# Performance work log

Measured on AMD Instinct MI355X. Metric: run time of the kernel, lower is better.

Reference implementation:

```python
import jax, jax.numpy as jnp
import numpy as np
from jax import lax

B, T, D, H, W = 2, 8, 64, 64, 64
E, HID = 4, 256


def _layernorm(x, g, b, eps=1e-5):
    m = x.mean(-1, keepdims=True)
    v = ((x - m) ** 2).mean(-1, keepdims=True)
    return (x - m) / jnp.sqrt(v + eps) * g + b


def _pscan(A, X, axis):
    # linear recurrence h_t = A_t * h_{t-1} + X_t via associative scan
    def comb(l, r):
        a1, x1 = l
        a2, x2 = r
        return a2 * a1, a2 * x1 + x2
    return lax.associative_scan(comb, (A, X), axis=axis)[1]


def setup_inputs() -> dict:
    key = jax.random.key(0)
    ks = jax.random.split(key, 32)
    r = lambda i, shape, s=1.0: jax.random.normal(ks[i], shape, jnp.float32) * s
    D2 = 2 * D
    return {
        'x_re': r(0, (B, T, D, H, W)), 'x_im': r(1, (B, T, D, H, W)),
        'dt': jax.random.uniform(ks[2], (T,), jnp.float32, 0.5, 1.0),
        'ln_s_g': jnp.ones(D2), 'ln_s_b': jnp.zeros(D2),
        'conv_w': r(3, (3, 3, D2, D2), 0.03), 'conv_b': jnp.zeros(D2),
        'mom_w': r(4, (D2, D2), 0.08), 'mom_b': jnp.zeros(D2),
        'adv_w': jnp.full((1,), 0.1, jnp.float32),
        'enc_re': r(5, (D, D), 0.1), 'enc_im': r(6, (D, D), 0.1),
        'dec_re': r(7, (D, D), 0.1), 'dec_im': r(8, (D, D), 0.1),
        'flux_a_re': r(9, (D,)), 'flux_a_im': r(10, (D,), 0.1),
        'fin_re': r(11, (D, D), 0.1), 'fin_im': r(12, (D, D), 0.1),
        'fproj_re': r(13, (D, D), 0.1), 'fproj_im': r(14, (D, D), 0.1),
        'gate_w': r(15, (D2, D), 0.1), 'gate_b': jnp.zeros(D),
        'lam_re': r(16, (D,)), 'lam_im': r(17, (D,), 0.1),
        'noise_re': r(18, (B, T, H, W, D)), 'noise_im': r(19, (B, T, H, W, D)),
        'e_scale': jnp.full((1,), 0.1, jnp.float32),
        'ln_t_g': jnp.ones(D2), 'ln_t_b': jnp.zeros(D2),
        'router_w': r(20, (D2, E), 0.1), 'router_b': jnp.zeros(E),
        'w1': r(21, (E, D2, HID), 0.08), 'b1': jnp.zeros((E, HID)),
        'w2': r(22, (E, HID, D2), 0.08), 'b2': jnp.zeros((E, D2)),
    }


def _forward(x_re, x_im, dt, ln_s_g, ln_s_b, conv_w, conv_b, mom_w, mom_b, adv_w,
             enc_re, enc_im, dec_re, dec_im, flux_a_re, flux_a_im, fin_re, fin_im,
             fproj_re, fproj_im, gate_w, gate_b, lam_re, lam_im, noise_re, noise_im,
             e_scale, ln_t_g, ln_t_b, router_w, router_b, w1, b1, w2, b2):
    x = (x_re + 1j * x_im).astype(jnp.complex64)            # [B,T,D,H,W]
    target_energy = (jnp.abs(x) ** 2).mean(axis=(-2, -1))   # [B,T,D]
    momentum = x.mean(axis=(-2, -1))                        # [B,T,D] complex
    xcl = jnp.transpose(x, (0, 1, 3, 4, 2))                 # [B,T,H,W,D]
    Bs, Ts, Hs, Ws, Ds = xcl.shape
    D2 = 2 * Ds
    # --- spatial complex (Clifford) conv branch: LN over 2D channels + conv ---
    xr = jnp.concatenate([xcl.real, xcl.imag], -1)          # [B,T,H,W,2D]
    xn = _layernorm(xr, ln_s_g, ln_s_b)
    y = lax.conv_general_dilated(xn.reshape(Bs * Ts, Hs, Ws, D2), conv_w,
                                 (1, 1), 'SAME',
                                 dimension_numbers=('NHWC', 'HWIO', 'NHWC')) + conv_b
    y = y.reshape(Bs, Ts, Hs, Ws, D2)
    xcl = xcl + (y[..., :Ds] + 1j * y[..., Ds:])
    # --- momentum advection ---
    z_mean = xcl.mean(axis=(2, 3))                          # [B,T,D]
    mom_cat = jnp.concatenate([momentum.real, momentum.imag], -1) @ mom_w + mom_b
    mom_new = mom_cat[..., :Ds] + 1j * mom_cat[..., Ds:]
    dtb = jnp.broadcast_to(dt[None, :], (Bs, Ts))
    xcl = xcl + (mom_new * adv_w[0])[:, :, None, None, :] * dtb[:, :, None, None, None]
    momentum = 0.9 * momentum + 0.1 * z_mean
    # --- eigenbasis encode ---
    x_eigen = xcl @ (enc_re + 1j * enc_im)                  # [B,T,H,W,D]
    x_mean = x_eigen.mean(axis=(2, 3))                      # [B,T,D]
    # --- flux tracker: parallel scan over T ---
    A_flux = jnp.exp(-jax.nn.softplus(flux_a_re) + 1j * flux_a_im)
    A_flux = jnp.broadcast_to(A_flux, (Bs, Ts, Ds)).astype(jnp.complex64)
    X_flux = x_mean @ (fin_re + 1j * fin_im)
    flux_seq = _pscan(A_flux, X_flux, axis=1)               # [B,T,D]
    source = flux_seq @ (fproj_re + 1j * fproj_im)
    gate = jax.nn.sigmoid(jnp.concatenate([flux_seq.real, flux_seq.imag], -1) @ gate_w + gate_b)
    g = gate[:, :, None, None, :]
    forcing = x_eigen * g + source[:, :, None, None, :] * (1.0 - g)
    # --- temporal propagation: per-site parallel scan over T ---
    lam = -jax.nn.softplus(lam_re) + 1j * lam_im            # [D]
    op_decay = jnp.exp(lam[None, None, :] * dtb[:, :, None])  # [B,T,D]
    op_forcing = (op_decay - 1.0) / lam
    u_t = forcing * op_forcing[:, :, None, None, :]
    A_time = jnp.broadcast_to(op_decay[:, :, None, None, :], u_t.shape)
    u_out = _pscan(A_time, u_t, axis=1)                     # [B,T,H,W,D]
    noise = 0.01 * jnp.sqrt(dtb)[:, :, None, None, None] * (noise_re + 1j * noise_im)
    u_out = u_out + noise
    # --- decode + energy projection ---
    x_out = u_out @ (dec_re + 1j * dec_im)                  # [B,T,H,W,D]
    cur_e = (jnp.abs(x_out) ** 2).mean(axis=(2, 3))
    ratio = jnp.clip(target_energy / (cur_e + 1e-8), 0.5, 2.0)
    sf = jnp.sqrt(ratio)[:, :, None, None, :]
    x_out = x_out * (1.0 + e_scale[0] * (sf - 1.0))
    # --- temporal LN + MoE FFN on real-concat tokens ---
    xr2 = jnp.concatenate([x_out.real, x_out.imag], -1)
    xn2 = _layernorm(xr2, ln_t_g, ln_t_b)                   # [B,T,H,W,2D]
    tok = xn2.reshape(-1, D2)                               # [N,2D]
    p = jax.nn.softmax(tok @ router_w + router_b, -1)       # [N,E]
    hmid = jax.nn.gelu(jnp.einsum('nd,edh->neh', tok, w1) + b1)
    eout = jnp.einsum('neh,ehd->ned', hmid, w2) + b2
    out_tok = tok + jnp.einsum('ne,ned->nd', p, eout)
    out = out_tok.reshape(Bs, Ts, Hs, Ws, D2)
    x_out_c = out[..., :Ds] + 1j * out[..., Ds:]
    z_out = xcl + x_out_c
    z = jnp.transpose(z_out, (0, 1, 4, 2, 3))               # [B,T,D,H,W]
    return jnp.stack([z.real, z.imag])                      # [2,B,T,D,H,W]


def reference(x_re, x_im, dt, ln_s_g, ln_s_b, conv_w, conv_b, mom_w, mom_b, adv_w,
              enc_re, enc_im, dec_re, dec_im, flux_a_re, flux_a_im, fin_re, fin_im,
              fproj_re, fproj_im, gate_w, gate_b, lam_re, lam_im, noise_re, noise_im,
              e_scale, ln_t_g, ln_t_b, router_w, router_b, w1, b1, w2, b2):
    return _forward(x_re, x_im, dt, ln_s_g, ln_s_b, conv_w, conv_b, mom_w, mom_b, adv_w,
                    enc_re, enc_im, dec_re, dec_im, flux_a_re, flux_a_im, fin_re, fin_im,
                    fproj_re, fproj_im, gate_w, gate_b, lam_re, lam_im, noise_re, noise_im,
                    e_scale, ln_t_g, ln_t_b, router_w, router_b, w1, b1, w2, b2)
```

## Files before the change

kernel.cpp:

```cpp
#include <hip/hip_runtime.h>
#include <hip/hip_bf16.h>
#include <math.h>


#define W_C      8388608u
#define W_CWT    12582912u
#define W_W1T    14680064u
#define W_W2T    14745600u
#define W_ENCM   14811136u
#define W_DECM   14819328u
#define W_XMP_RE 14827520u
#define W_XMP_IM 14893056u
#define W_EP_RE  14958592u
#define W_EP_IM  15220736u
#define W_EIG_RE 16777216u
#define W_K1R    20971520u
#define W_K1I    21037056u
#define W_K1E    21102592u
#define W_SMALL  25165824u
#define W_TE     (W_SMALL+0u)
#define W_MTRE   (W_SMALL+3072u)
#define W_MTIM   (W_SMALL+4096u)
#define W_GATE   (W_SMALL+5120u)
#define W_SRCRE  (W_SMALL+6144u)
#define W_SRCIM  (W_SMALL+7168u)
#define W_OPFRE  (W_SMALL+8192u)
#define W_OPFIM  (W_SMALL+9216u)
#define W_OPDRE  (W_SMALL+10240u)
#define W_OPDIM  (W_SMALL+11264u)
#define W_SCALE  (W_SMALL+12288u)

#define XB_IM 4194304u

typedef __attribute__((ext_vector_type(8))) short bf16x8;
typedef __attribute__((ext_vector_type(4))) float f32x4;

__device__ __forceinline__ unsigned short bfr(float x) {
  __hip_bfloat16 h = __float2bfloat16(x);
  return *(unsigned short*)&h;
}
__device__ __forceinline__ unsigned int pk2(float a, float b) {
  return ((unsigned int)bfr(b) << 16) | (unsigned int)bfr(a);
}
__device__ __forceinline__ float sb2f(short s) {
  return __uint_as_float(((unsigned int)(unsigned short)s) << 16);
}

__global__ __launch_bounds__(256) void k2_transpose_ln(
    const float* __restrict__ xre, const float* __restrict__ xim,
    const float* __restrict__ g, const float* __restrict__ bb_, float* ws) {
  int blk = blockIdx.x; int bt = blk >> 6, h = blk & 63;
  __shared__ float tre[64][65], tim[64][65];
  __shared__ float ps[4][64], pq[4][64], pe[4][64];
  __shared__ float mean_l[64], rstd_l[64];
  size_t inbase = (size_t)bt * 262144 + (size_t)h * 64;
  for (int i = threadIdx.x; i < 1024; i += 256) {
    int d = i >> 4, w4 = (i & 15) * 4;
    float4 vr = *(const float4*)&xre[inbase + (size_t)d * 4096 + w4];
    float4 vi = *(const float4*)&xim[inbase + (size_t)d * 4096 + w4];
    tre[d][w4] = vr.x; tre[d][w4 + 1] = vr.y; tre[d][w4 + 2] = vr.z; tre[d][w4 + 3] = vr.w;
    tim[d][w4] = vi.x; tim[d][w4 + 1] = vi.y; tim[d][w4 + 2] = vi.z; tim[d][w4 + 3] = vi.w;
  }
  __syncthreads();
  {
    int w = threadIdx.x & 63, part = threadIdx.x >> 6;
    float s = 0.f, sq = 0.f;
    for (int dd = part * 16; dd < part * 16 + 16; dd++) {
      float vr = tre[dd][w], vi = tim[dd][w];
      s += vr + vi; sq += vr * vr + vi * vi;
    }
    ps[part][w] = s; pq[part][w] = sq;
  }
  __syncthreads();
  if (threadIdx.x < 64) {
    int w = threadIdx.x;
    float s  = ps[0][w] + ps[1][w] + ps[2][w] + ps[3][w];
    float sq = pq[0][w] + pq[1][w] + pq[2][w] + pq[3][w];
    float m = s / 128.f;
    float v = sq / 128.f - m * m;
    mean_l[w] = m; rstd_l[w] = rsqrtf(v + 1e-5f);
  }
  __syncthreads();
  {
    int d = threadIdx.x & 63, part = threadIdx.x >> 6;
    float sr = 0.f, si = 0.f, se = 0.f;
    for (int w = part * 16; w < part * 16 + 16; w++) {
      float vr = tre[d][w], vi = tim[d][w];
      sr += vr; si += vi; se += vr * vr + vi * vi;
    }
    ps[part][d] = sr; pq[part][d] = si; pe[part][d] = se;
  }
  __syncthreads();
  if (threadIdx.x < 64) {
    int d = threadIdx.x;
    int idx = h * 1024 + bt * 64 + d;
    ws[W_K1R + idx] = ps[0][d] + ps[1][d] + ps[2][d] + ps[3][d];
    ws[W_K1I + idx] = pq[0][d] + pq[1][d] + pq[2][d] + pq[3][d];
    ws[W_K1E + idx] = pe[0][d] + pe[1][d] + pe[2][d] + pe[3][d];
  }
  size_t tokbase = (size_t)blk * 64;
  __hip_bfloat16* xnb = (__hip_bfloat16*)(ws + W_C);
  int c0 = (threadIdx.x & 63) * 2, wg = threadIdx.x >> 6;
  float gc0 = g[c0], bc0 = bb_[c0], gc1 = g[c0 + 1], bc1 = bb_[c0 + 1];
  for (int pass = 0; pass < 16; pass++) {
    int w = pass * 4 + wg;
    float m = mean_l[w], rs = rstd_l[w];
    float v0 = (c0 < 64) ? tre[c0][w] : tim[c0 - 64][w];
    float v1 = (c0 + 1 < 64) ? tre[c0 + 1][w] : tim[c0 + 1 - 64][w];
    *(unsigned int*)&xnb[tokbase * 128 + (size_t)w * 128 + c0] =
        pk2((v0 - m) * rs * gc0 + bc0, (v1 - m) * rs * gc1 + bc1);
  }
}

__global__ void k1b2b(const float* __restrict__ mom_w, const float* __restrict__ mom_b,
                      const float* __restrict__ adv_w, const float* __restrict__ dt, float* ws) {
  int bt = blockIdx.x; int t = bt & 7;
  __shared__ float mc[128], outl[128];
  int tid = threadIdx.x;
  if (tid < 64) {
    int d = tid;
    float a = 0.f, b = 0.f, c = 0.f;
    for (int h = 0; h < 64; h++) {
      int idx = h * 1024 + bt * 64 + d;
      a += ws[W_K1R + idx]; b += ws[W_K1I + idx]; c += ws[W_K1E + idx];
    }
    ws[W_TE + bt * 64 + d] = c / 4096.f;
    mc[d] = a / 4096.f;
    mc[64 + d] = b / 4096.f;
  }
  __syncthreads();
  float acc = mom_b[tid];
  for (int k = 0; k < 128; k++) acc += mc[k] * mom_w[k * 128 + tid];
  outl[tid] = acc;
  __syncthreads();
  if (tid < 64) {
    float f = adv_w[0] * dt[t];
    ws[W_MTRE + bt * 64 + tid] = outl[tid] * f;
    ws[W_MTIM + bt * 64 + tid] = outl[64 + tid] * f;
  }
}

__global__ void k0_wprep(const float* __restrict__ w1, const float* __restrict__ w2,
                         const float* __restrict__ cw,
                         const float* __restrict__ enc_re, const float* __restrict__ enc_im,
                         const float* __restrict__ dec_re, const float* __restrict__ dec_im,
                         float* ws) {
  __hip_bfloat16* w1f = (__hip_bfloat16*)(ws + W_W1T);
  __hip_bfloat16* w2f = (__hip_bfloat16*)(ws + W_W2T);
  __hip_bfloat16* cwt = (__hip_bfloat16*)(ws + W_CWT);
  __hip_bfloat16* encM = (__hip_bfloat16*)(ws + W_ENCM);
  __hip_bfloat16* decM = (__hip_bfloat16*)(ws + W_DECM);
  int idx = blockIdx.x * 256 + threadIdx.x;
  if (idx < 131072) {
    {
      int j = idx & 7, lane = (idx >> 3) & 63, kt = (idx >> 9) & 3, nt = (idx >> 11) & 15, e = idx >> 15;
      int cout = nt * 16 + (lane & 15);
      int cin = kt * 32 + (lane >> 4) * 8 + j;
      w1f[idx] = __float2bfloat16(w1[((size_t)(e * 128 + cin)) * 256 + cout]);
    }
    {
      int j = idx & 7, lane = (idx >> 3) & 63, kt = (idx >> 9) & 7, nt = (idx >> 12) & 7, e = idx >> 15;
      int cout = nt * 16 + (lane & 15);
      int cin = kt * 32 + (lane >> 4) * 8 + j;
      w2f[idx] = __float2bfloat16(w2[((size_t)(e * 256 + cin)) * 128 + cout]);
    }
  }
  if (idx < 147456) {
    int j = idx & 7, lane = (idx >> 3) & 63, kt = (idx >> 9) & 3, r = idx >> 11;
    int nt = r & 7, tap = r >> 3;
    int cout = nt * 16 + (lane & 15);
    int cin = kt * 32 + (lane >> 4) * 8 + j;
    cwt[idx] = __float2bfloat16(cw[((size_t)(tap * 128 + cin)) * 128 + cout]);
  }
  if (idx < 16384) {
    int jj = idx & 7, lane = (idx >> 3) & 63, kt = (idx >> 9) & 3, nt = idx >> 11;
    int jc = nt * 16 + (lane & 15);
    int k = kt * 32 + (lane >> 4) * 8 + jj;
    float ve, vd;
    if (k < 64) {
      ve = (jc < 64) ? enc_re[k * 64 + jc] : enc_im[k * 64 + (jc - 64)];
      vd = (jc < 64) ? dec_re[k * 64 + jc] : dec_im[k * 64 + (jc - 64)];
    } else {
      int kk = k - 64;
      ve = (jc < 64) ? -enc_im[kk * 64 + jc] : enc_re[kk * 64 + (jc - 64)];
      vd = (jc < 64) ? -dec_im[kk * 64 + jc] : dec_re[kk * 64 + (jc - 64)];
    }
    encM[idx] = __float2bfloat16(ve);
    decM[idx] = __float2bfloat16(vd);
  }
}

__global__ __launch_bounds__(256) void k3_conv_enc(
    const float* __restrict__ xre, const float* __restrict__ xim,
    const float* __restrict__ cb, float* ws) {
  int blk = blockIdx.x; int bt = blk >> 6, h = blk & 63;
  const __hip_bfloat16* xnb = (const __hip_bfloat16*)(ws + W_C);
  const __hip_bfloat16* cwt = (const __hip_bfloat16*)(ws + W_CWT);
  const __hip_bfloat16* encM = (const __hip_bfloat16*)(ws + W_ENCM);
  __hip_bfloat16* xclb = (__hip_bfloat16*)ws;
  __hip_bfloat16* eigb = (__hip_bfloat16*)(ws + W_EIG_RE);
  __shared__ __align__(16) char smem[3 * 66 * 136 * 2];
  __hip_bfloat16 (*xin)[66][136] = (__hip_bfloat16(*)[66][136])smem;
  char* A = smem;
  int tid = threadIdx.x, lane = tid & 63, wv = tid >> 6;
  int arow = lane & 15, kgrp = (lane >> 4) * 8, rbase = (lane >> 4) * 4;

  for (int r = 0; r < 3; r++) {
    int hh = h + r - 1;
    if (hh < 0 || hh >= 64) {
      unsigned int* z = (unsigned int*)&xin[r][0][0];
      for (int i = tid; i < 4488; i += 256) z[i] = 0u;
    } else {
      if (tid < 68) *(unsigned int*)&xin[r][0][tid * 2] = 0u;
      else if (tid < 136) *(unsigned int*)&xin[r][65][(tid - 136 + 68) * 2] = 0u;
      const __hip_bfloat16* src = xnb + ((size_t)bt * 4096 + (size_t)hh * 64) * 128;
      for (int i = tid; i < 1024; i += 256) {
        int wp = (i >> 4) + 1, c8 = (i & 15) * 8;
        *(bf16x8*)&xin[r][wp][c8] = *(const bf16x8*)&src[(size_t)(wp - 1) * 128 + c8];
      }
    }
  }
  __syncthreads();

  f32x4 oacc[4][2];
  #pragma unroll
  for (int m = 0; m < 4; m++) {
    oacc[m][0] = (f32x4){0.f, 0.f, 0.f, 0.f};
    oacc[m][1] = (f32x4){0.f, 0.f, 0.f, 0.f};
  }

  for (int tap = 0; tap < 9; tap++) {
    int kh = tap / 3, kw = tap % 3;
    const __hip_bfloat16* wt0 = cwt + ((size_t)(tap * 8 + wv * 2) * 4) * 512 + lane * 8;
    #pragma unroll
    for (int kt = 0; kt < 4; kt++) {
      bf16x8 a[4];
      #pragma unroll
      for (int m = 0; m < 4; m++)
        a[m] = *(const bf16x8*)&xin[kh][m * 16 + arow + kw][kt * 32 + kgrp];
      bf16x8 b0 = *(const bf16x8*)&wt0[(size_t)kt * 512];
      bf16x8 b1 = *(const bf16x8*)&wt0[(size_t)(kt + 4) * 512];
      #pragma unroll
      for (int m = 0; m < 4; m++) {
        oacc[m][0] = __builtin_amdgcn_mfma_f32_16x16x32_bf16(a[m], b0, oacc[m][0], 0, 0, 0);
        oacc[m][1] = __builtin_amdgcn_mfma_f32_16x16x32_bf16(a[m], b1, oacc[m][1], 0, 0, 0);
      }
    }
  }
  __syncthreads();

  size_t rowtok = (size_t)blk * 64;
  #pragma unroll
  for (int n = 0; n < 2; n++) {
    int cout = (wv * 2 + n) * 16 + arow;
    bool isre = cout < 64;
    int d = cout & 63;
    float add = cb[cout] + ws[(isre ? W_MTRE : W_MTIM) + bt * 64 + d];
    size_t xb = isre ? 0u : XB_IM;
    const float* xsrc = (isre ? xre : xim) + ((size_t)(bt * 64 + d) * 64 + h) * 64;
    #pragma unroll
    for (int m = 0; m < 4; m++) {
      float4 xv = *(const float4*)&xsrc[m * 16 + rbase];
      #pragma unroll
      for (int r = 0; r < 4; r++) {
        int w = m * 16 + rbase + r;
        float xo = (r == 0) ? xv.x : (r == 1) ? xv.y : (r == 2) ? xv.z : xv.w;
        float v = xo + oacc[m][n][r] + add;
        xclb[xb + (rowtok + w) * 64 + d] = __float2bfloat16(v);
        *(__hip_bfloat16*)(A + w * 256 + ((cout * 2) ^ ((w & 7) << 4))) = __float2bfloat16(v);
      }
    }
  }
  __syncthreads();

  f32x4 acc[4][2];
  #pragma unroll
  for (int m = 0; m < 4; m++) {
    acc[m][0] = (f32x4){0.f, 0.f, 0.f, 0.f};
    acc[m][1] = (f32x4){0.f, 0.f, 0.f, 0.f};
  }
  #pragma unroll
  for (int kt = 0; kt < 4; kt++) {
    bf16x8 a[4];
    #pragma unroll
    for (int m = 0; m < 4; m++)
      a[m] = *(const bf16x8*)(A + (m * 16 + arow) * 256 + (((kt * 32 + kgrp) * 2) ^ ((arow & 7) << 4)));
    bf16x8 b0 = *(const bf16x8*)&encM[(((size_t)(wv * 2 + 0) * 4 + kt) * 64 + lane) * 8];
    bf16x8 b1 = *(const bf16x8*)&encM[(((size_t)(wv * 2 + 1) * 4 + kt) * 64 + lane) * 8];
    #pragma unroll
    for (int m = 0; m < 4; m++) {
      acc[m][0] = __builtin_amdgcn_mfma_f32_16x16x32_bf16(a[m], b0, acc[m][0], 0, 0, 0);
      acc[m][1] = __builtin_amdgcn_mfma_f32_16x16x32_bf16(a[m], b1, acc[m][1], 0, 0, 0);
    }
  }
  #pragma unroll
  for (int n = 0; n < 2; n++) {
    int jc = (wv * 2 + n) * 16 + arow;
    size_t eb = (jc < 64) ? 0u : XB_IM;
    int col = jc & 63;
    #pragma unroll
    for (int m = 0; m < 4; m++)
      #pragma unroll
      for (int r = 0; r < 4; r++)
        eigb[eb + (rowtok + m * 16 + rbase + r) * 64 + col] = __float2bfloat16(acc[m][n][r]);
    float s = 0.f;
    #pragma unroll
    for (int m = 0; m < 4; m++)
      #pragma unroll
      for (int r = 0; r < 4; r++) s += acc[m][n][r];
    s += __shfl_xor(s, 16);
    s += __shfl_xor(s, 32);
    if (lane < 16)
      ws[(jc < 64 ? W_XMP_RE : W_XMP_IM) + (size_t)blk * 64 + col] = s;
  }
}

__device__ __forceinline__ float softplusf(float x) {
  return (x > 20.f) ? x : log1pf(expf(x));
}

__global__ void k6_seq(const float* __restrict__ fin_re, const float* __restrict__ fin_im,
                       const float* __restrict__ fproj_re, const float* __restrict__ fproj_im,
                       const float* __restrict__ flux_a_re, const float* __restrict__ flux_a_im,
                       const float* __restrict__ gate_w, const float* __restrict__ gate_b,
                       const float* __restrict__ lam_re, const float* __restrict__ lam_im,
                       const float* __restrict__ dt, float* ws) {
  __shared__ float xmr[1024], xmi[1024], Xfr[1024], Xfi[1024], flr[1024], fli[1024];
  int tid = threadIdx.x;
  for (int i = tid; i < 1024; i += 256) {
    int bt = i >> 6, j = i & 63;
    float sr = 0.f, si = 0.f;
    for (int q = 0; q < 64; q++) {
      sr += ws[W_XMP_RE + (size_t)(bt * 64 + q) * 64 + j];
      si += ws[W_XMP_IM + (size_t)(bt * 64 + q) * 64 + j];
    }
    xmr[i] = sr / 4096.f; xmi[i] = si / 4096.f;
  }
  __syncthreads();
  for (int i = tid; i < 1024; i += 256) {
    int bt = i >> 6, j = i & 63;
    float ar = 0.f, ai = 0.f;
    for (int d = 0; d < 64; d++) {
      float xr = xmr[bt * 64 + d], xi = xmi[bt * 64 + d];
      float wr = fin_re[d * 64 + j], wi = fin_im[d * 64 + j];
      ar += xr * wr - xi * wi; ai += xr * wi + xi * wr;
    }
    Xfr[i] = ar; Xfi[i] = ai;
  }
  __syncthreads();
  if (tid < 128) {
    int b = tid >> 6, j = tid & 63;
    float mag = expf(-softplusf(flux_a_re[j]));
    float aar = mag * cosf(flux_a_im[j]), aai = mag * sinf(flux_a_im[j]);
    float sr = 0.f, si = 0.f;
    for (int t = 0; t < 8; t++) {
      int idx = (b * 8 + t) * 64 + j;
      float nr = aar * sr - aai * si + Xfr[idx];
      float ni = aar * si + aai * sr + Xfi[idx];
      sr = nr; si = ni;
      flr[idx] = sr; fli[idx] = si;
    }
  }
  __syncthreads();
  for (int i = tid; i < 1024; i += 256) {
    int bt = i >> 6, j = i & 63;
    float ar = 0.f, ai = 0.f, lg = 0.f;
    for (int d = 0; d < 64; d++) {
      float fr = flr[bt * 64 + d], fi = fli[bt * 64 + d];
      float wr = fproj_re[d * 64 + j], wi = fproj_im[d * 64 + j];
      ar += fr * wr - fi * wi; ai += fr * wi + fi * wr;
      lg += fr * gate_w[d * 64 + j] + fi * gate_w[(64 + d) * 64 + j];
    }
    ws[W_SRCRE + i] = ar; ws[W_SRCIM + i] = ai;
    ws[W_GATE + i] = 1.f / (1.f + expf(-(lg + gate_b[j])));
  }
  for (int i = tid; i < 1024; i += 256) {
    int bt = i >> 6, d = i & 63, t = bt & 7;
    float lr = -softplusf(lam_re[d]), li = lam_im[d];
    float dtv = dt[t];
    float mag = expf(lr * dtv);
    float dr = mag * cosf(li * dtv), di = mag * sinf(li * dtv);
    ws[W_OPDRE + i] = dr; ws[W_OPDIM + i] = di;
    float omr = dr - 1.f, omi = di;
    float den = lr * lr + li * li;
    ws[W_OPFRE + i] = (omr * lr + omi * li) / den;
    ws[W_OPFIM + i] = (omi * lr - omr * li) / den;
  }
}

__global__ __launch_bounds__(256) void k7_dec(const float* __restrict__ nre,
                                              const float* __restrict__ nim,
                                              const float* __restrict__ dt, float* ws) {
  int blk = blockIdx.x;
  int b = blk >> 8, h = (blk >> 2) & 63, wq = blk & 3;
  const __hip_bfloat16* decM = (const __hip_bfloat16*)(ws + W_DECM);
  __hip_bfloat16* eigb = (__hip_bfloat16*)(ws + W_EIG_RE);
  __shared__ float gl[8][64], srl[8][64], sil[8][64], ofr[8][64], ofi[8][64], odr[8][64], odi[8][64];
  __shared__ __align__(16) char A[2][4096];
  __shared__ float dts[8];
  int tid = threadIdx.x, lane = tid & 63, wv = tid >> 6;
  int arow = lane & 15, kgrp = (lane >> 4) * 8, rbase = (lane >> 4) * 4;
  for (int i = tid; i < 512; i += 256) {
    int t = i >> 6, d = i & 63, idx = (b * 8 + t) * 64 + d;
    gl[t][d]  = ws[W_GATE + idx];
    srl[t][d] = ws[W_SRCRE + idx]; sil[t][d] = ws[W_SRCIM + idx];
    ofr[t][d] = ws[W_OPFRE + idx]; ofi[t][d] = ws[W_OPFIM + idx];
    odr[t][d] = ws[W_OPDRE + idx]; odi[t][d] = ws[W_OPDIM + idx];
  }
  if (tid < 8) dts[tid] = dt[tid];
  __syncthreads();

  int dp = (tid & 31) * 2, wslot = tid >> 5;
  float ur[2][2], ui[2][2];
  #pragma unroll
  for (int a_ = 0; a_ < 2; a_++) { ur[a_][0] = 0.f; ur[a_][1] = 0.f; ui[a_][0] = 0.f; ui[a_][1] = 0.f; }

  for (int t = 0; t < 8; t++) {
    float ns = 0.01f * sqrtf(dts[t]);
    size_t tokb = ((size_t)(b * 8 + t) * 64 + h) * 64 + (size_t)wq * 16;
    char* At = A[t & 1];
    float g0 = gl[t][dp],  g1 = gl[t][dp + 1];
    float s0 = srl[t][dp], s1 = srl[t][dp + 1];
    float q0 = sil[t][dp], q1 = sil[t][dp + 1];
    float f0 = ofr[t][dp], f1 = ofr[t][dp + 1];
    float e0 = ofi[t][dp], e1 = ofi[t][dp + 1];
    float r0 = odr[t][dp], r1 = odr[t][dp + 1];
    float o0 = odi[t][dp], o1 = odi[t][dp + 1];
    #pragma unroll
    for (int wi = 0; wi < 2; wi++) {
      int wl = wslot + wi * 8;
      size_t off = (tokb + wl) * 64 + dp;
      unsigned int re2 = *(const unsigned int*)&eigb[off];
      unsigned int im2 = *(const unsigned int*)&eigb[XB_IM + off];
      float2 nr2 = *(const float2*)&nre[off];
      float2 ni2 = *(const float2*)&nim[off];
      float uo0, vo0, uo1, vo1;
      {
        float er_ = __uint_as_float(re2 << 16);
        float ei_ = __uint_as_float(im2 << 16);
        float fre = er_ * g0 + s0 * (1.f - g0);
        float fim = ei_ * g0 + q0 * (1.f - g0);
        float utr = fre * f0 - fim * e0;
        float uti = fre * e0 + fim * f0;
        float nur = r0 * ur[wi][0] - o0 * ui[wi][0] + utr;
        float nui = r0 * ui[wi][0] + o0 * ur[wi][0] + uti;
        ur[wi][0] = nur; ui[wi][0] = nui;
        uo0 = nur + ns * nr2.x; vo0 = nui + ns * ni2.x;
      }
      {
        float er_ = __uint_as_float(re2 & 0xffff0000u);
        float ei_ = __uint_as_float(im2 & 0xffff0000u);
        float fre = er_ * g1 + s1 * (1.f - g1);
        float fim = ei_ * g1 + q1 * (1.f - g1);
        float utr = fre * f1 - fim * e1;
        float uti = fre * e1 + fim * f1;
        float nur = r1 * ur[wi][1] - o1 * ui[wi][1] + utr;
        float nui = r1 * ui[wi][1] + o1 * ur[wi][1] + uti;
        ur[wi][1] = nur; ui[wi][1] = nui;
        uo1 = nur + ns * nr2.y; vo1 = nui + ns * ni2.y;
      }
      int sw = (wl & 7) << 4;
      *(unsigned int*)(At + wl * 256 + ((dp * 2) ^ sw)) = pk2(uo0, uo1);
      *(unsigned int*)(At + wl * 256 + ((128 + dp * 2) ^ sw)) = pk2(vo0, vo1);
    }
    __syncthreads();
    f32x4 acc[2];
    acc[0] = (f32x4){0.f, 0.f, 0.f, 0.f};
    acc[1] = (f32x4){0.f, 0.f, 0.f, 0.f};
    #pragma unroll
    for (int kt = 0; kt < 4; kt++) {
      bf16x8 a0 = *(const bf16x8*)(At + arow * 256 + (((kt * 32 + kgrp) * 2) ^ ((arow & 7) << 4)));
      bf16x8 b0 = *(const bf16x8*)&decM[(((size_t)(wv * 2 + 0) * 4 + kt) * 64 + lane) * 8];
      bf16x8 b1 = *(const bf16x8*)&decM[(((size_t)(wv * 2 + 1) * 4 + kt) * 64 + lane) * 8];
      acc[0] = __builtin_amdgcn_mfma_f32_16x16x32_bf16(a0, b0, acc[0], 0, 0, 0);
      acc[1] = __builtin_amdgcn_mfma_f32_16x16x32_bf16(a0, b1, acc[1], 0, 0, 0);
    }
    #pragma unroll
    for (int n = 0; n < 2; n++) {
      int jc = (wv * 2 + n) * 16 + arow;
      size_t eb = (jc < 64) ? 0u : XB_IM;
      int col = jc & 63;
      #pragma unroll
      for (int r = 0; r < 4; r++)
        eigb[eb + (tokb + rbase + r) * 64 + col] = __float2bfloat16(acc[n][r]);
      float s = acc[n][0] * acc[n][0] + acc[n][1] * acc[n][1]
              + acc[n][2] * acc[n][2] + acc[n][3] * acc[n][3];
      s += __shfl_xor(s, 16);
      s += __shfl_xor(s, 32);
      if (lane < 16)
        ws[(jc < 64 ? W_EP_RE : W_EP_IM)
           + (size_t)((b * 8 + t) * 256 + h * 4 + wq) * 64 + col] = s;
    }
  }
}

__global__ void k9b_scale(const float* __restrict__ escale, float* ws) {
  int bt = blockIdx.x; int j = threadIdx.x;
  float s = 0.f;
  for (int q = 0; q < 256; q++) {
    size_t idx = (size_t)(bt * 256 + q) * 64 + j;
    s += ws[W_EP_RE + idx] + ws[W_EP_IM + idx];
  }
  float cur = s / 4096.f;
  float te = ws[W_TE + bt * 64 + j];
  float ratio = te / (cur + 1e-8f);
  ratio = fminf(fmaxf(ratio, 0.5f), 2.0f);
  ws[W_SCALE + bt * 64 + j] = 1.f + escale[0] * (sqrtf(ratio) - 1.f);
}

__global__ __launch_bounds__(512) void k11_moe(
    const float* __restrict__ rw, const float* __restrict__ rb,
    const float* __restrict__ b1, const float* __restrict__ b2,
    const float* __restrict__ g2, const float* __restrict__ b2_,
    float* __restrict__ ws, float* __restrict__ out) {
  int blk = blockIdx.x; int bt = blk >> 6, h = blk & 63;
  const __hip_bfloat16* w1f = (const __hip_bfloat16*)(ws + W_W1T);
  const __hip_bfloat16* w2f = (const __hip_bfloat16*)(ws + W_W2T);
  const __hip_bfloat16* xclb = (const __hip_bfloat16*)ws;
  const __hip_bfloat16* eigb = (const __hip_bfloat16*)(ws + W_EIG_RE);
  __shared__ __align__(16) char smem[81920];
  __shared__ float pl[64][4];
  __shared__ float sc[64];
  __shared__ float mean_l[64], rstd_l[64];
  char* lt = smem;
  float (*obuf)[129] = (float(*)[129])smem;
  float* psq = (float*)(smem + 16384);
  int tid = threadIdx.x, lane = tid & 63, wv = tid >> 6;
  int arow = lane & 15, kgrp = (lane >> 4) * 8, rbase = (lane >> 4) * 4;
  size_t tokbase = (size_t)blk * 64;

  if (tid < 64) sc[tid] = ws[W_SCALE + bt * 64 + tid];
  __syncthreads();

  int w = tid >> 3, part = tid & 7;
  int c0 = part * 16, dbase = (part & 3) * 16;
  const __hip_bfloat16* rp = eigb + ((part < 4) ? 0u : XB_IM) + (tokbase + w) * 64 + dbase;
  float4 vv[4];
  {
    bf16x8 h0 = *(const bf16x8*)rp;
    bf16x8 h1 = *(const bf16x8*)(rp + 8);
    float f[16];
    #pragma unroll
    for (int j = 0; j < 8; j++) { f[j] = sb2f(h0[j]); f[8 + j] = sb2f(h1[j]); }
    float s = 0.f, sq = 0.f;
    #pragma unroll
    for (int q = 0; q < 4; q++) {
      float4 t4;
      t4.x = f[q * 4 + 0] * sc[dbase + q * 4 + 0];
      t4.y = f[q * 4 + 1] * sc[dbase + q * 4 + 1];
      t4.z = f[q * 4 + 2] * sc[dbase + q * 4 + 2];
      t4.w = f[q * 4 + 3] * sc[dbase + q * 4 + 3];
      vv[q] = t4;
      s  += t4.x + t4.y + t4.z + t4.w;
      sq += t4.x * t4.x + t4.y * t4.y + t4.z * t4.z + t4.w * t4.w;
    }
    psq[part * 64 + w] = s;
    psq[512 + part * 64 + w] = sq;
  }
  __syncthreads();
  if (tid < 64) {
    float s = 0.f, sq = 0.f;
    #pragma unroll
    for (int p = 0; p < 8; p++) { s += psq[p * 64 + tid]; sq += psq[512 + p * 64 + tid]; }
    float m = s / 128.f, v = sq / 128.f - m * m;
    mean_l[tid] = m; rstd_l[tid] = rsqrtf(v + 1e-5f);
  }
  __syncthreads();
  {
    float m = mean_l[w], rs = rstd_l[w];
    int szw = (w & 7) << 4;
    #pragma unroll
    for (int q = 0; q < 4; q++) {
      int c = c0 + q * 4;
      float a0 = (vv[q].x - m) * rs * g2[c]     + b2_[c];
      float a1 = (vv[q].y - m) * rs * g2[c + 1] + b2_[c + 1];
      float a2 = (vv[q].z - m) * rs * g2[c + 2] + b2_[c + 2];
      float a3 = (vv[q].w - m) * rs * g2[c + 3] + b2_[c + 3];
      *(unsigned int*)(lt + w * 256 + ((c * 2) ^ szw)) = pk2(a0, a1);
      *(unsigned int*)(lt + w * 256 + (((c + 2) * 2) ^ szw)) = pk2(a2, a3);
    }
  }
  __syncthreads();
  if (tid < 256) {
    int l = tid >> 2, e = tid & 3;
    float acc = rb[e];
    const float* rwe = rw + e;
    int sz = (l & 7) << 4;
    for (int dd = 0; dd < 128; dd += 2) {
      unsigned int u = *(const unsigned int*)(lt + l * 256 + ((dd * 2) ^ sz));
      float x0 = __uint_as_float(u << 16);
      float x1 = __uint_as_float(u & 0xffff0000u);
      acc += x0 * rwe[dd * 4] + x1 * rwe[dd * 4 + 4];
    }
    pl[l][e] = acc;
  }
  __syncthreads();
  if (tid < 64) {
    float m = fmaxf(fmaxf(pl[tid][0], pl[tid][1]), fmaxf(pl[tid][2], pl[tid][3]));
    float e0 = expf(pl[tid][0] - m), e1 = expf(pl[tid][1] - m);
    float e2 = expf(pl[tid][2] - m), e3 = expf(pl[tid][3] - m);
    float s = e0 + e1 + e2 + e3;
    float rs = __builtin_amdgcn_rcpf(s);
    pl[tid][0] = e0 * rs; pl[tid][1] = e1 * rs; pl[tid][2] = e2 * rs; pl[tid][3] = e3 * rs;
  }

  f32x4 oacc[4];
  #pragma unroll
  for (int m = 0; m < 4; m++) {
    int col = wv * 16 + arow;
    oacc[m] = (f32x4){0.f, 0.f, 0.f, 0.f};
    #pragma unroll
    for (int r = 0; r < 4; r++) {
      int row = m * 16 + rbase + r;
      oacc[m][r] = __bfloat162float(
          *(const __hip_bfloat16*)(lt + row * 256 + ((col * 2) ^ ((row & 7) << 4))));
    }
  }
  __syncthreads();

  for (int e = 0; e < 4; e++) {
    char* hb = smem + 16384 + (e & 1) * 32768;
    f32x4 acc1[4][2];
    #pragma unroll
    for (int m = 0; m < 4; m++) {
      acc1[m][0] = (f32x4){0.f, 0.f, 0.f, 0.f};
      acc1[m][1] = (f32x4){0.f, 0.f, 0.f, 0.f};
    }
    #pragma unroll
    for (int kt = 0; kt < 4; kt++) {
      bf16x8 a[4];
      #pragma unroll
      for (int m = 0; m < 4; m++) {
        int row = m * 16 + arow;
        a[m] = *(const bf16x8*)(lt + row * 256 + (((kt * 32 + kgrp) * 2) ^ ((arow & 7) << 4)));
      }
      bf16x8 b0 = *(const bf16x8*)&w1f[(((size_t)(e * 16 + wv * 2 + 0) * 4 + kt) * 64 + lane) * 8];
      bf16x8 b1 = *(const bf16x8*)&w1f[(((size_t)(e * 16 + wv * 2 + 1) * 4 + kt) * 64 + lane) * 8];
      #pragma unroll
      for (int m = 0; m < 4; m++) {
        acc1[m][0] = __builtin_amdgcn_mfma_f32_16x16x32_bf16(a[m], b0, acc1[m][0], 0, 0, 0);
        acc1[m][1] = __builtin_amdgcn_mfma_f32_16x16x32_bf16(a[m], b1, acc1[m][1], 0, 0, 0);
      }
    }
    #pragma unroll
    for (int n = 0; n < 2; n++) {
      int col = (wv * 2 + n) * 16 + arow;
      float bv = b1[e * 256 + col];
      #pragma unroll
      for (int m = 0; m < 4; m++)
        #pragma unroll
        for (int r = 0; r < 4; r++) {
          float hv = acc1[m][n][r] + bv;
          float z = 1.5957691216f * hv + 0.0713548162f * hv * hv * hv;
          float gelu = hv * __builtin_amdgcn_rcpf(1.f + __expf(-z));
          int row = m * 16 + rbase + r;
          *(__hip_bfloat16*)(hb + row * 512 + ((col * 2) ^ ((row & 7) << 4))) =
              __float2bfloat16(gelu);
        }
    }
    __syncthreads();
    f32x4 acc2[4];
    #pragma unroll
    for (int m = 0; m < 4; m++) acc2[m] = (f32x4){0.f, 0.f, 0.f, 0.f};
    #pragma unroll
    for (int kt = 0; kt < 8; kt++) {
      bf16x8 a2[4];
      #pragma unroll
      for (int m = 0; m < 4; m++) {
        int row = m * 16 + arow;
        a2[m] = *(const bf16x8*)(hb + row * 512 + (((kt * 32 + kgrp) * 2) ^ ((arow & 7) << 4)));
      }
      bf16x8 bb = *(const bf16x8*)&w2f[(((size_t)(e * 8 + wv) * 8 + kt) * 64 + lane) * 8];
      #pragma unroll
      for (int m = 0; m < 4; m++)
        acc2[m] = __builtin_amdgcn_mfma_f32_16x16x32_bf16(a2[m], bb, acc2[m], 0, 0, 0);
    }
    {
      int col = wv * 16 + arow;
      float bv2 = b2[e * 128 + col];
      #pragma unroll
      for (int m = 0; m < 4; m++)
        #pragma unroll
        for (int r = 0; r < 4; r++)
          oacc[m][r] += pl[m * 16 + rbase + r][e] * (acc2[m][r] + bv2);
    }
  }

  __syncthreads();
  #pragma unroll
  for (int m = 0; m < 4; m++) {
    int col = wv * 16 + arow;
    #pragma unroll
    for (int r = 0; r < 4; r++)
      obuf[m * 16 + rbase + r][col] = oacc[m][r];
  }
  __syncthreads();

  for (int i = tid; i < 4096; i += 512) {
    int wt = i >> 6, c0r = (i & 63) * 2;
    size_t xb = (c0r < 64) ? 0u : XB_IM;
    int dd = c0r & 63;
    unsigned int u = *(const unsigned int*)&xclb[xb + (tokbase + wt) * 64 + dd];
    obuf[wt][c0r]     += __uint_as_float(u << 16);
    obuf[wt][c0r + 1] += __uint_as_float(u & 0xffff0000u);
  }
  __syncthreads();
  for (int i = tid; i < 8192; i += 512) {
    int d2 = i >> 6, wt = i & 63;
    out[(size_t)(d2 >> 6) * 4194304 + (size_t)bt * 262144 + (size_t)(d2 & 63) * 4096
        + (size_t)h * 64 + wt] = obuf[wt][d2];
  }
}

extern "C" void kernel_launch(void* const* d_in, const int* in_sizes, int n_in,
                              void* d_out, int out_size, void* d_ws, size_t ws_size,
                              hipStream_t stream) {
  const float* x_re      = (const float*)d_in[0];
  const float* x_im      = (const float*)d_in[1];
  const float* dt        = (const float*)d_in[2];
  const float* ln_s_g    = (const float*)d_in[3];
  const float* ln_s_b    = (const float*)d_in[4];
  const float* conv_w    = (const float*)d_in[5];
  const float* conv_b    = (const float*)d_in[6];
  const float* mom_w     = (const float*)d_in[7];
  const float* mom_b     = (const float*)d_in[8];
  const float* adv_w     = (const float*)d_in[9];
  const float* enc_re    = (const float*)d_in[10];
  const float* enc_im    = (const float*)d_in[11];
  const float* dec_re    = (const float*)d_in[12];
  const float* dec_im    = (const float*)d_in[13];
  const float* flux_a_re = (const float*)d_in[14];
  const float* flux_a_im = (const float*)d_in[15];
  const float* fin_re    = (const float*)d_in[16];
  const float* fin_im    = (const float*)d_in[17];
  const float* fproj_re  = (const float*)d_in[18];
  const float* fproj_im  = (const float*)d_in[19];
  const float* gate_w    = (const float*)d_in[20];
  const float* gate_b    = (const float*)d_in[21];
  const float* lam_re    = (const float*)d_in[22];
  const float* lam_im    = (const float*)d_in[23];
  const float* noise_re  = (const float*)d_in[24];
  const float* noise_im  = (const float*)d_in[25];
  const float* e_scale   = (const float*)d_in[26];
  const float* ln_t_g    = (const float*)d_in[27];
  const float* ln_t_b    = (const float*)d_in[28];
  const float* router_w  = (const float*)d_in[29];
  const float* router_b  = (const float*)d_in[30];
  const float* w1        = (const float*)d_in[31];
  const float* b1        = (const float*)d_in[32];
  const float* w2        = (const float*)d_in[33];
  const float* b2        = (const float*)d_in[34];
  float* ws  = (float*)d_ws;
  float* out = (float*)d_out;

  k0_wprep<<<576, 256, 0, stream>>>(w1, w2, conv_w, enc_re, enc_im, dec_re, dec_im, ws);
  k2_transpose_ln<<<1024, 256, 0, stream>>>(x_re, x_im, ln_s_g, ln_s_b, ws);
  k1b2b<<<16, 128, 0, stream>>>(mom_w, mom_b, adv_w, dt, ws);
  k3_conv_enc<<<1024, 256, 0, stream>>>(x_re, x_im, conv_b, ws);
  k6_seq<<<1, 256, 0, stream>>>(fin_re, fin_im, fproj_re, fproj_im, flux_a_re, flux_a_im,
                                gate_w, gate_b, lam_re, lam_im, dt, ws);
  k7_dec<<<512, 256, 0, stream>>>(noise_re, noise_im, dt, ws);
  k9b_scale<<<16, 64, 0, stream>>>(e_scale, ws);
  k11_moe<<<1024, 512, 0, stream>>>(router_w, router_b, b1, b2, ln_t_g, ln_t_b, ws, out);
}
```

Measured before the change: 243.3 us.

## Fuse layernorm and router via wave shuffles; write MoE output directly from registers

Reads the per-channel scale straight from global memory and reduces the layernorm statistics and the router logits with xor-shuffles across the 8 threads that share a token. This removes the shared-memory partial-sum buffers and several block-wide barriers, and the softmax is computed redundantly in registers. The epilogue adds the bf16 residual per lane and stores float4 results straight to global memory, dropping the shared-memory transpose buffer and its barriers. In exchange the residual reads are scattered 2-byte gathers, and the barrier after the initial oacc read is removed. That removal relies on the first expert's writes landing in a different smem region than lt.

```diff
diff --git a/kernel.cpp b/kernel.cpp
--- a/kernel.cpp
+++ b/kernel.cpp
@@ -520,89 +520,64 @@
   const __hip_bfloat16* eigb = (const __hip_bfloat16*)(ws + W_EIG_RE);
   __shared__ __align__(16) char smem[81920];
   __shared__ float pl[64][4];
-  __shared__ float sc[64];
-  __shared__ float mean_l[64], rstd_l[64];
   char* lt = smem;
-  float (*obuf)[129] = (float(*)[129])smem;
-  float* psq = (float*)(smem + 16384);
   int tid = threadIdx.x, lane = tid & 63, wv = tid >> 6;
   int arow = lane & 15, kgrp = (lane >> 4) * 8, rbase = (lane >> 4) * 4;
   size_t tokbase = (size_t)blk * 64;
 
-  if (tid < 64) sc[tid] = ws[W_SCALE + bt * 64 + tid];
-  __syncthreads();
-
   int w = tid >> 3, part = tid & 7;
   int c0 = part * 16, dbase = (part & 3) * 16;
   const __hip_bfloat16* rp = eigb + ((part < 4) ? 0u : XB_IM) + (tokbase + w) * 64 + dbase;
-  float4 vv[4];
+  const float* scg = ws + W_SCALE + bt * 64 + dbase;
+  float an[16];
   {
     bf16x8 h0 = *(const bf16x8*)rp;
     bf16x8 h1 = *(const bf16x8*)(rp + 8);
     float f[16];
     #pragma unroll
-    for (int j = 0; j < 8; j++) { f[j] = sb2f(h0[j]); f[8 + j] = sb2f(h1[j]); }
+    for (int j = 0; j < 8; j++) {
+      f[j]     = sb2f(h0[j]) * scg[j];
+      f[8 + j] = sb2f(h1[j]) * scg[8 + j];
+    }
     float s = 0.f, sq = 0.f;
     #pragma unroll
-    for (int q = 0; q < 4; q++) {
-      float4 t4;
-      t4.x = f[q * 4 + 0] * sc[dbase + q * 4 + 0];
-      t4.y = f[q * 4 + 1] * sc[dbase + q * 4 + 1];
-      t4.z = f[q * 4 + 2] * sc[dbase + q * 4 + 2];
-      t4.w = f[q * 4 + 3] * sc[dbase + q * 4 + 3];
-      vv[q] = t4;
-      s  += t4.x + t4.y + t4.z + t4.w;
-      sq += t4.x * t4.x + t4.y * t4.y + t4.z * t4.z + t4.w * t4.w;
-    }
-    psq[part * 64 + w] = s;
-    psq[512 + part * 64 + w] = sq;
-  }
-  __syncthreads();
-  if (tid < 64) {
-    float s = 0.f, sq = 0.f;
-    #pragma unroll
-    for (int p = 0; p < 8; p++) { s += psq[p * 64 + tid]; sq += psq[512 + p * 64 + tid]; }
+    for (int k = 0; k < 16; k++) { s += f[k]; sq += f[k] * f[k]; }
+    s  += __shfl_xor(s, 1);  s  += __shfl_xor(s, 2);  s  += __shfl_xor(s, 4);
+    sq += __shfl_xor(sq, 1); sq += __shfl_xor(sq, 2); sq += __shfl_xor(sq, 4);
     float m = s / 128.f, v = sq / 128.f - m * m;
-    mean_l[tid] = m; rstd_l[tid] = rsqrtf(v + 1e-5f);
-  }
-  __syncthreads();
-  {
-    float m = mean_l[w], rs = rstd_l[w];
+    float rstd = rsqrtf(v + 1e-5f);
     int szw = (w & 7) << 4;
     #pragma unroll
     for (int q = 0; q < 4; q++) {
       int c = c0 + q * 4;
-      float a0 = (vv[q].x - m) * rs * g2[c]     + b2_[c];
-      float a1 = (vv[q].y - m) * rs * g2[c + 1] + b2_[c + 1];
-      float a2 = (vv[q].z - m) * rs * g2[c + 2] + b2_[c + 2];
-      float a3 = (vv[q].w - m) * rs * g2[c + 3] + b2_[c + 3];
+      float a0 = (f[q * 4 + 0] - m) * rstd * g2[c]     + b2_[c];
+      float a1 = (f[q * 4 + 1] - m) * rstd * g2[c + 1] + b2_[c + 1];
+      float a2 = (f[q * 4 + 2] - m) * rstd * g2[c + 2] + b2_[c + 2];
+      float a3 = (f[q * 4 + 3] - m) * rstd * g2[c + 3] + b2_[c + 3];
+      an[q * 4 + 0] = a0; an[q * 4 + 1] = a1; an[q * 4 + 2] = a2; an[q * 4 + 3] = a3;
       *(unsigned int*)(lt + w * 256 + ((c * 2) ^ szw)) = pk2(a0, a1);
       *(unsigned int*)(lt + w * 256 + (((c + 2) * 2) ^ szw)) = pk2(a2, a3);
     }
-  }
-  __syncthreads();
-  if (tid < 256) {
-    int l = tid >> 2, e = tid & 3;
-    float acc = rb[e];
-    const float* rwe = rw + e;
-    int sz = (l & 7) << 4;
-    for (int dd = 0; dd < 128; dd += 2) {
-      unsigned int u = *(const unsigned int*)(lt + l * 256 + ((dd * 2) ^ sz));
-      float x0 = __uint_as_float(u << 16);
-      float x1 = __uint_as_float(u & 0xffff0000u);
-      acc += x0 * rwe[dd * 4] + x1 * rwe[dd * 4 + 4];
-    }
-    pl[l][e] = acc;
-  }
-  __syncthreads();
-  if (tid < 64) {
-    float m = fmaxf(fmaxf(pl[tid][0], pl[tid][1]), fmaxf(pl[tid][2], pl[tid][3]));
-    float e0 = expf(pl[tid][0] - m), e1 = expf(pl[tid][1] - m);
-    float e2 = expf(pl[tid][2] - m), e3 = expf(pl[tid][3] - m);
-    float s = e0 + e1 + e2 + e3;
-    float rs = __builtin_amdgcn_rcpf(s);
-    pl[tid][0] = e0 * rs; pl[tid][1] = e1 * rs; pl[tid][2] = e2 * rs; pl[tid][3] = e3 * rs;
-  }
+    float l0 = 0.f, l1 = 0.f, l2 = 0.f, l3 = 0.f;
+    #pragma unroll
+    for (int k = 0; k < 16; k++) {
+      float4 r4 = *(const float4*)&rw[(c0 + k) * 4];
+      l0 += an[k] * r4.x; l1 += an[k] * r4.y; l2 += an[k] * r4.z; l3 += an[k] * r4.w;
+    }
+    l0 += __shfl_xor(l0, 1); l0 += __shfl_xor(l0, 2); l0 += __shfl_xor(l0, 4);
+    l1 += __shfl_xor(l1, 1); l1 += __shfl_xor(l1, 2); l1 += __shfl_xor(l1, 4);
+    l2 += __shfl_xor(l2, 1); l2 += __shfl_xor(l2, 2); l2 += __shfl_xor(l2, 4);
+    l3 += __shfl_xor(l3, 1); l3 += __shfl_xor(l3, 2); l3 += __shfl_xor(l3, 4);
+    l0 += rb[0]; l1 += rb[1]; l2 += rb[2]; l3 += rb[3];
+    float mx = fmaxf(fmaxf(l0, l1), fmaxf(l2, l3));
+    float e0 = expf(l0 - mx), e1 = expf(l1 - mx), e2 = expf(l2 - mx), e3 = expf(l3 - mx);
+    float rs = __builtin_amdgcn_rcpf(e0 + e1 + e2 + e3);
+    if (part == 0) {
+      float4 p; p.x = e0 * rs; p.y = e1 * rs; p.z = e2 * rs; p.w = e3 * rs;
+      *(float4*)&pl[w][0] = p;
+    }
+  }
+  __syncthreads();
 
   f32x4 oacc[4];
   #pragma unroll
@@ -616,7 +591,6 @@
           *(const __hip_bfloat16*)(lt + row * 256 + ((col * 2) ^ ((row & 7) << 4))));
     }
   }
-  __syncthreads();
 
   for (int e = 0; e < 4; e++) {
     char* hb = smem + 16384 + (e & 1) * 32768;
@@ -686,29 +660,23 @@
     }
   }
 
-  __syncthreads();
-  #pragma unroll
-  for (int m = 0; m < 4; m++) {
+  {
     int col = wv * 16 + arow;
-    #pragma unroll
-    for (int r = 0; r < 4; r++)
-      obuf[m * 16 + rbase + r][col] = oacc[m][r];
-  }
-  __syncthreads();
-
-  for (int i = tid; i < 4096; i += 512) {
-    int wt = i >> 6, c0r = (i & 63) * 2;
-    size_t xb = (c0r < 64) ? 0u : XB_IM;
-    int dd = c0r & 63;
-    unsigned int u = *(const unsigned int*)&xclb[xb + (tokbase + wt) * 64 + dd];
-    obuf[wt][c0r]     += __uint_as_float(u << 16);
-    obuf[wt][c0r + 1] += __uint_as_float(u & 0xffff0000u);
-  }
-  __syncthreads();
-  for (int i = tid; i < 8192; i += 512) {
-    int d2 = i >> 6, wt = i & 63;
-    out[(size_t)(d2 >> 6) * 4194304 + (size_t)bt * 262144 + (size_t)(d2 & 63) * 4096
-        + (size_t)h * 64 + wt] = obuf[wt][d2];
+    size_t xb = (col < 64) ? 0u : XB_IM;
+    int dd = col & 63;
+    size_t obase = (size_t)(col >> 6) * 4194304 + (size_t)bt * 262144
+                 + (size_t)dd * 4096 + (size_t)h * 64;
+    #pragma unroll
+    for (int m = 0; m < 4; m++) {
+      int wtb = m * 16 + rbase;
+      float4 v;
+      #pragma unroll
+      for (int r = 0; r < 4; r++) {
+        float res = __bfloat162float(xclb[xb + (tokbase + wtb + r) * 64 + dd]);
+        ((float*)&v)[r] = oacc[m][r] + res;
+      }
+      *(float4*)&out[obase + wtb] = v;
+    }
   }
 }
 
```

Measured after the change: 241.7 us. No clear change (-0.6%).
